# Optimization experiments

Measured on AMD Instinct MI355X. Metric: run time of the kernel, lower is better.

## Reference

```python
import jax, jax.numpy as jnp
import numpy as np


def setup_inputs() -> dict:
    key = jax.random.key(0)
    k1, k2, k3 = jax.random.split(key, 3)
    B, H, W, D, K = 16, 32, 32, 128, 32
    x = jax.random.normal(k1, (B, H, W, D), dtype=jnp.float32)
    std = 1.0 / (K * D) ** 0.5
    codewords = jax.random.uniform(k2, (K, D), minval=-std, maxval=std, dtype=jnp.float32)
    scale = jax.random.uniform(k3, (K,), minval=-1.0, maxval=0.0, dtype=jnp.float32)
    return {"x": x, "codewords": codewords, "scale": scale}


def reference(x, codewords, scale):
    B, H, W, D = x.shape
    K = codewords.shape[0]
    X = x.reshape(B, H * W, D)                      # [B, N, D]
    # scaled squared distances: s_k * ||x_n - c_k||^2 via expansion (no BNKD tensor)
    x2 = jnp.sum(X * X, axis=-1, keepdims=True)     # [B, N, 1]
    c2 = jnp.sum(codewords * codewords, axis=-1)    # [K]
    xc = jnp.einsum('bnd,kd->bnk', X, codewords)    # [B, N, K]
    SL = scale[None, None, :] * (x2 - 2.0 * xc + c2[None, None, :])
    A = jax.nn.softmax(SL, axis=2)                  # assignment weights [B, N, K]
    # E_bk = sum_n A_bnk * (x_bn - c_k)
    E = jnp.einsum('bnk,bnd->bkd', A, X) - jnp.sum(A, axis=1)[:, :, None] * codewords[None]
    return E
```

## Files before the change

### kernel.cpp

```cpp
#include <hip/hip_runtime.h>


typedef __attribute__((ext_vector_type(8))) short bf16x8;
typedef __attribute__((ext_vector_type(16))) float f32x16;

constexpr int XBS = 136;
constexpr int AST = 40;

__device__ __forceinline__ unsigned short f2bf(float f) {
    unsigned u = __float_as_uint(f);
    u += 0x7fffu + ((u >> 16) & 1u);
    return (unsigned short)(u >> 16);
}
__device__ __forceinline__ float bf2f(unsigned short h) {
    return __uint_as_float((unsigned)h << 16);
}

__global__ __launch_bounds__(256)
void enc_partial(const float* __restrict__ x, const float* __restrict__ cw,
                 const float* __restrict__ scale, float* __restrict__ out)
{
    __shared__ unsigned short xb_s[32 * XBS];
    __shared__ unsigned short cb_s[32 * XBS];
    __shared__ unsigned short At_s[32 * AST];
    __shared__ float x2_s[32], c2_s[32];
    __shared__ float asum_s[4 * 32];
    __shared__ float asumf_s[32];

    const int tid = threadIdx.x;
    const int b   = blockIdx.x >> 5;
    const int s   = blockIdx.x & 31;
    const int lc  = tid & 31;
    const int lh  = (tid >> 5) & 1;
    const int w   = tid >> 6;

    const float4* xg4 = (const float4*)(x + (size_t)(b * 1024 + s * 32) * 128);
    const float4* cg4 = (const float4*)cw;

#pragma unroll
    for (int i = 0; i < 4; ++i) {
        const int f   = tid + 256 * i;
        const int row = 8 * i + (tid >> 5);
        const int col = tid & 31;
        float4 vx = xg4[f];
        float4 vc = cg4[f];
        short4 hx = { (short)f2bf(vx.x), (short)f2bf(vx.y),
                      (short)f2bf(vx.z), (short)f2bf(vx.w) };
        short4 hc = { (short)f2bf(vc.x), (short)f2bf(vc.y),
                      (short)f2bf(vc.z), (short)f2bf(vc.w) };
        *(short4*)&xb_s[row * XBS + col * 4] = hx;
        *(short4*)&cb_s[row * XBS + col * 4] = hc;
        float sx = vx.x * vx.x + vx.y * vx.y + vx.z * vx.z + vx.w * vx.w;
        float sc = vc.x * vc.x + vc.y * vc.y + vc.z * vc.z + vc.w * vc.w;
#pragma unroll
        for (int m = 16; m >= 1; m >>= 1) {
            sx += __shfl_xor(sx, m);
            sc += __shfl_xor(sc, m);
        }
        if (col == 0) { x2_s[row] = sx; c2_s[row] = sc; }
    }
    __syncthreads();

    f32x16 acc;
#pragma unroll
    for (int i = 0; i < 16; ++i) acc[i] = 0.f;
#pragma unroll
    for (int t = 0; t < 8; ++t) {
        bf16x8 af  = *(const bf16x8*)&xb_s[lc * XBS + t * 16 + lh * 8];
        bf16x8 bfr = *(const bf16x8*)&cb_s[lc * XBS + t * 16 + lh * 8];
        acc = __builtin_amdgcn_mfma_f32_32x32x16_bf16(af, bfr, acc, 0, 0, 0);
    }

    {
        const float sck = scale[lc];
        const float c2k = c2_s[lc];
        const float4 x2v = *(const float4*)&x2_s[8 * w + 4 * lh];
        float sl[4] = {
            sck * (x2v.x - 2.f * acc[4 * w + 0] + c2k),
            sck * (x2v.y - 2.f * acc[4 * w + 1] + c2k),
            sck * (x2v.z - 2.f * acc[4 * w + 2] + c2k),
            sck * (x2v.w - 2.f * acc[4 * w + 3] + c2k) };
        float a[4];
#pragma unroll
        for (int q = 0; q < 4; ++q) {
            float m = sl[q];
#pragma unroll
            for (int msk = 16; msk >= 1; msk >>= 1) m = fmaxf(m, __shfl_xor(m, msk));
            float e = __expf(sl[q] - m);
            float den = e;
#pragma unroll
            for (int msk = 16; msk >= 1; msk >>= 1) den += __shfl_xor(den, msk);
            a[q] = e / den;
        }
        short4 ha = { (short)f2bf(a[0]), (short)f2bf(a[1]),
                      (short)f2bf(a[2]), (short)f2bf(a[3]) };
        *(short4*)&At_s[lc * AST + 8 * w + 4 * lh] = ha;
        float ap = (a[0] + a[1]) + (a[2] + a[3]);
        ap += __shfl_xor(ap, 32);
        if (lh == 0) asum_s[w * 32 + lc] = ap;
    }
    __syncthreads();

    if (tid < 32)
        asumf_s[tid] = (asum_s[tid] + asum_s[32 + tid]) +
                       (asum_s[64 + tid] + asum_s[96 + tid]);

    f32x16 e;
#pragma unroll
    for (int i = 0; i < 16; ++i) e[i] = 0.f;
#pragma unroll
    for (int t = 0; t < 2; ++t) {
        bf16x8 af = *(const bf16x8*)&At_s[lc * AST + t * 16 + lh * 8];
        const int nb = t * 16 + lh * 8;
        bf16x8 bfr;
#pragma unroll
        for (int j = 0; j < 8; ++j)
            bfr[j] = (short)xb_s[(nb + j) * XBS + w * 32 + lc];
        e = __builtin_amdgcn_mfma_f32_32x32x16_bf16(af, bfr, e, 0, 0, 0);
    }
    __syncthreads();

    {
        float* ob = out + (size_t)b * 4096;
        const int dd = w * 32 + lc;
#pragma unroll
        for (int r = 0; r < 16; ++r) {
            const int kk = (r & 3) + 8 * (r >> 2) + 4 * lh;
            float v = e[r] - asumf_s[kk] * bf2f(cb_s[kk * XBS + dd]);
            unsafeAtomicAdd(&ob[kk * 128 + dd], v);
        }
    }
}

extern "C" void kernel_launch(void* const* d_in, const int* in_sizes, int n_in,
                              void* d_out, int out_size, void* d_ws, size_t ws_size,
                              hipStream_t stream)
{
    const float* x     = (const float*)d_in[0];
    const float* cw    = (const float*)d_in[1];
    const float* scale = (const float*)d_in[2];
    float* out = (float*)d_out;

    hipMemsetAsync(out, 0, (size_t)16 * 32 * 128 * sizeof(float), stream);
    enc_partial<<<512, 256, 0, stream>>>(x, cw, scale, out);
}
```

Baseline: 72.67 us.

## Replace global atomics and memset with bf16 workspace partials plus reduce kernel

Each block now writes its partial E tile as bf16 into a workspace slot instead of doing float atomic adds into the output, and a second kernel sums the 32 slice partials per batch. This removes the memset launch and atomic contention on the output. In exchange it adds a kernel launch and workspace traffic, and storing partials in bf16 loses some precision.

```diff
diff --git a/kernel.cpp b/kernel.cpp
--- a/kernel.cpp
+++ b/kernel.cpp
@@ -18,7 +18,7 @@
 
 __global__ __launch_bounds__(256)
 void enc_partial(const float* __restrict__ x, const float* __restrict__ cw,
-                 const float* __restrict__ scale, float* __restrict__ out)
+                 const float* __restrict__ scale, unsigned short* __restrict__ ws)
 {
     __shared__ unsigned short xb_s[32 * XBS];
     __shared__ unsigned short cb_s[32 * XBS];
@@ -121,14 +121,52 @@
     __syncthreads();
 
     {
-        float* ob = out + (size_t)b * 4096;
+        unsigned short* wb = ws + (size_t)(b * 32 + s) * 4096;
         const int dd = w * 32 + lc;
 #pragma unroll
         for (int r = 0; r < 16; ++r) {
             const int kk = (r & 3) + 8 * (r >> 2) + 4 * lh;
             float v = e[r] - asumf_s[kk] * bf2f(cb_s[kk * XBS + dd]);
-            unsafeAtomicAdd(&ob[kk * 128 + dd], v);
+            wb[kk * 128 + dd] = f2bf(v);
         }
+    }
+}
+
+__global__ __launch_bounds__(256)
+void enc_reduce(const unsigned short* __restrict__ ws, float* __restrict__ out)
+{
+    __shared__ float red_s[3][256];
+
+    const int tid  = threadIdx.x;
+    const int lane = tid & 63;
+    const int sg   = tid >> 6;
+    const int b    = blockIdx.x >> 4;
+    const int q    = (blockIdx.x & 15) * 64 + lane;
+    const unsigned short* base = ws + (size_t)b * 131072 + q * 4;
+
+    float4 a0 = {0,0,0,0}, a1 = {0,0,0,0};
+#pragma unroll
+    for (int s = 0; s < 8; s += 2) {
+        ushort4 v0 = *(const ushort4*)&base[(sg * 8 + s + 0) * 4096];
+        ushort4 v1 = *(const ushort4*)&base[(sg * 8 + s + 1) * 4096];
+        a0.x += bf2f(v0.x); a0.y += bf2f(v0.y); a0.z += bf2f(v0.z); a0.w += bf2f(v0.w);
+        a1.x += bf2f(v1.x); a1.y += bf2f(v1.y); a1.z += bf2f(v1.z); a1.w += bf2f(v1.w);
+    }
+    float4 a;
+    a.x = a0.x + a1.x; a.y = a0.y + a1.y; a.z = a0.z + a1.z; a.w = a0.w + a1.w;
+
+    if (sg) *(float4*)&red_s[sg - 1][lane * 4] = a;
+    __syncthreads();
+    if (sg == 0) {
+        float4 r0 = *(const float4*)&red_s[0][lane * 4];
+        float4 r1 = *(const float4*)&red_s[1][lane * 4];
+        float4 r2 = *(const float4*)&red_s[2][lane * 4];
+        float4 r;
+        r.x = (a.x + r0.x) + (r1.x + r2.x);
+        r.y = (a.y + r0.y) + (r1.y + r2.y);
+        r.z = (a.z + r0.z) + (r1.z + r2.z);
+        r.w = (a.w + r0.w) + (r1.w + r2.w);
+        *(float4*)&out[(size_t)b * 4096 + q * 4] = r;
     }
 }
 
@@ -140,7 +178,8 @@
     const float* cw    = (const float*)d_in[1];
     const float* scale = (const float*)d_in[2];
     float* out = (float*)d_out;
+    unsigned short* ws = (unsigned short*)d_ws;
 
-    hipMemsetAsync(out, 0, (size_t)16 * 32 * 128 * sizeof(float), stream);
-    enc_partial<<<512, 256, 0, stream>>>(x, cw, scale, out);
+    enc_partial<<<512, 256, 0, stream>>>(x, cw, scale, ws);
+    enc_reduce<<<256, 256, 0, stream>>>(ws, out);
 }
```

Result: faster. 67.17 us (-7.6%).
